# Performance work log

Hardware: AMD Instinct MI355X
Metric: run time of the kernel (lower is better)

## Reference

```python
import jax, jax.numpy as jnp
import numpy as np

N = 50000      # nodes
E = 800000     # edges (avg degree 16)
DIN = 256      # input_dim
DH = 128       # hidden_dim
ALPHA_LOGIT = 0.6190392084062235  # logit(0.65)


def setup_inputs() -> dict:
    key = jax.random.key(0)
    ks = jax.random.split(key, 12)
    f = lambda k, s: jax.random.normal(k, s, dtype=jnp.float32)
    return {
        "x": f(ks[0], (N, DIN)),
        "edge_index": jax.random.randint(ks[1], (2, E), 0, N, dtype=jnp.int32),
        "reranker_scores": f(ks[2], (N,)),
        # input_proj
        "Wp": f(ks[3], (DIN, DH)) * 0.02, "bp": jnp.zeros((DH,), jnp.float32),
        # SAGEConv 0: lin_l (aggregated neighbors, with bias), lin_r (root, no bias)
        "Wl0": f(ks[4], (DIN, DH)) * 0.02, "bl0": jnp.zeros((DH,), jnp.float32),
        "Wr0": f(ks[5], (DIN, DH)) * 0.02,
        # SAGEConv 1
        "Wl1": f(ks[6], (DH, DH)) * 0.02, "bl1": jnp.zeros((DH,), jnp.float32),
        "Wr1": f(ks[7], (DH, DH)) * 0.02,
        # score head MLP
        "W1": f(ks[8], (DH, DH // 2)) * 0.02, "b1": jnp.zeros((DH // 2,), jnp.float32),
        "W2": f(ks[9], (DH // 2, 1)) * 0.02, "b2": jnp.zeros((1,), jnp.float32),
        "alpha_logit": jnp.float32(ALPHA_LOGIT),
    }


def _sage_conv(h, src, dst, Wl, bl, Wr):
    # PyG SAGEConv (aggr='mean', root_weight=True):
    # out = lin_l(mean_{j in N(i)} h_j) + lin_r(h_i)
    msg = h[src]                                             # [E, d] gather
    agg = jax.ops.segment_sum(msg, dst, num_segments=N)      # [N, d]
    cnt = jax.ops.segment_sum(jnp.ones((src.shape[0],), h.dtype), dst, num_segments=N)
    agg = agg / jnp.maximum(cnt, 1.0)[:, None]               # mean; isolated nodes -> 0
    return agg @ Wl + bl + h @ Wr


def reference(x, edge_index, reranker_scores, Wp, bp, Wl0, bl0, Wr0,
              Wl1, bl1, Wr1, W1, b1, W2, b2, alpha_logit):
    src, dst = edge_index[0], edge_index[1]
    # norm_type='none' -> no input normalization; eval mode -> dropout is identity
    residual = x @ Wp + bp                                   # [N, DH]
    h = jax.nn.relu(_sage_conv(x, src, dst, Wl0, bl0, Wr0)) + residual
    h = jax.nn.relu(_sage_conv(h, src, dst, Wl1, bl1, Wr1)) + h
    gnn_scores = (jax.nn.relu(h @ W1 + b1) @ W2 + b2)[:, 0]  # [N]
    alpha = jax.nn.sigmoid(alpha_logit)
    return alpha * reranker_scores + (1.0 - alpha) * gnn_scores
```

## Files before the change

### kernel.cpp

```cpp
#include <hip/hip_runtime.h>
#include <hip/hip_bf16.h>


#define DIN 256
#define DH 128
#define NPB 512
#define NBMAX 128
#define EPB 2048
#define JL (EPB/256)
#define CAP 12288
#define SLOTS 16384

typedef __attribute__((ext_vector_type(8))) short short8;
typedef __attribute__((ext_vector_type(4))) float float4v;
typedef __attribute__((ext_vector_type(2))) float float2v;

__device__ inline ushort f2b(float f){
  unsigned u = __float_as_uint(f);
  u = (u + 0x7fffu + ((u >> 16) & 1u)) >> 16;
  return (ushort)u;
}
__device__ inline float blo(unsigned v){ return __uint_as_float(v << 16); }
__device__ inline float bhi(unsigned v){ return __uint_as_float(v & 0xffff0000u); }
__device__ inline short8 pack8(float4 f0, float4 f1){
  short8 v;
  v[0]=(short)f2b(f0.x); v[1]=(short)f2b(f0.y); v[2]=(short)f2b(f0.z); v[3]=(short)f2b(f0.w);
  v[4]=(short)f2b(f1.x); v[5]=(short)f2b(f1.y); v[6]=(short)f2b(f1.z); v[7]=(short)f2b(f1.w);
  return v;
}
__device__ inline void glds16(const ushort* g, ushort* l){
  __builtin_amdgcn_global_load_lds((const __attribute__((address_space(1))) void*)g,
                                   (__attribute__((address_space(3))) void*)l, 16, 0, 0);
}
__device__ inline unsigned char enc8(float v){
  return (unsigned char)(__builtin_amdgcn_cvt_pk_fp8_f32(v, v, 0, false) & 0xFF);
}
__device__ inline float2v dec8(unsigned u){
  return __builtin_amdgcn_cvt_pk_f32_fp8((int)u, false);
}

__device__ inline void gather16x2(const ushort* __restrict__ a8,
    const int* __restrict__ adj, int pA, int eA, int pB, int eB, int lane,
    float& a0A, float& a1A, float& a0B, float& a1B)
{
  while (pA < eA || pB < eB){
    ushort uA[16], uB[16];
    bool dA = pA < eA, dB = pB < eB;
    if (dA){
      #pragma unroll
      for (int j=0;j<16;j++) uA[j] = a8[(size_t)adj[pA+j]*64 + lane];
    }
    if (dB){
      #pragma unroll
      for (int j=0;j<16;j++) uB[j] = a8[(size_t)adj[pB+j]*64 + lane];
    }
    if (dA){
      #pragma unroll
      for (int j=0;j<16;j++){ float2v f = dec8(uA[j]); a0A += f[0]; a1A += f[1]; }
      pA += 16;
    }
    if (dB){
      #pragma unroll
      for (int j=0;j<16;j++){ float2v f = dec8(uB[j]); a0B += f[0]; a1B += f[1]; }
      pB += 16;
    }
  }
}

__global__ __launch_bounds__(256) void fused_front(
    const float* __restrict__ x, int N, ushort* __restrict__ xb, int nstripe,
    const float* __restrict__ Wp, const float* __restrict__ Wl0, const float* __restrict__ Wr0,
    const float* __restrict__ Wl1, const float* __restrict__ Wr1, const float* __restrict__ W1,
    ushort* __restrict__ Wpf, ushort* __restrict__ Wl0f, ushort* __restrict__ Wr0f,
    ushort* __restrict__ Wl1f, ushort* __restrict__ Wr1f, ushort* __restrict__ W1f,
    const int* __restrict__ src, const int* __restrict__ dst, int E, int NB,
    int* __restrict__ bucketCnt, int* __restrict__ pairS, int* __restrict__ pairD,
    int nPart, int nConv)
{
  __shared__ int hist[NBMAX], lbase[NBMAX], gbase[NBMAX], lcur[NBMAX], sc[NBMAX];
  __shared__ int ls[EPB], ld[EPB];
  int bid = blockIdx.x;
  int t = threadIdx.x;

  if (bid < nPart){
    int base = bid * EPB;
    int cntE = E - base; if (cntE > EPB) cntE = EPB;
    for (int i=t;i<NB;i+=256) hist[i]=0;
    __syncthreads();
    int myS[JL], myD[JL];
    #pragma unroll
    for (int j=0;j<JL;j++){
      int e = base + j*256 + t;
      if (e < E){ myS[j]=src[e]; myD[j]=dst[e]; atomicAdd(&hist[myD[j]>>9],1); }
      else myD[j] = -1;
    }
    __syncthreads();
    if (t < NBMAX) sc[t] = (t < NB)? hist[t] : 0;
    __syncthreads();
    for (int st=1; st<NBMAX; st<<=1){
      int v = 0;
      if (t < NBMAX && t >= st) v = sc[t-st];
      __syncthreads();
      if (t < NBMAX) sc[t] += v;
      __syncthreads();
    }
    if (t < NB){
      int excl = (t>0)? sc[t-1] : 0;
      lbase[t] = excl; lcur[t] = excl;
      gbase[t] = atomicAdd(&bucketCnt[t], hist[t]);
    }
    __syncthreads();
    #pragma unroll
    for (int j=0;j<JL;j++){
      if (myD[j] >= 0){
        int b = myD[j] >> 9;
        int p = atomicAdd(&lcur[b], 1);
        ls[p] = myS[j]; ld[p] = myD[j];
      }
    }
    __syncthreads();
    for (int i=t;i<cntE;i+=256){
      int d = ld[i];
      int b = d >> 9;
      int p = gbase[b] + (i - lbase[b]);
      if (p < SLOTS){
        pairS[(size_t)b*SLOTS + p] = ls[i];
        pairD[(size_t)b*SLOTS + p] = d;
      }
    }
  } else if (bid < nPart + nConv){
    int gi = (bid - nPart)*256 + t;
    if (gi < nstripe*512){
      int L = gi & 63, ks = (gi>>6)&7, s = gi>>9;
      int row = s*16 + (L&15);
      int k = ks*32 + (L>>4)*8;
      short8 v;
      if (row < N){
        const float* p = x + (size_t)row*DIN + k;
        v = pack8(*(const float4*)p, *(const float4*)(p+4));
      } else {
        #pragma unroll
        for (int j=0;j<8;j++) v[j]=0;
      }
      *(short8*)(xb + (size_t)gi*8) = v;
    }
  } else {
    int gi = (bid - nPart - nConv)*256 + t;
    if (gi < 17408){
      const float* sw; ushort* dw; int cols, b0;
      if      (gi <  4096){ sw=Wp;  dw=Wpf;  cols=128; b0=0; }
      else if (gi <  8192){ sw=Wl0; dw=Wl0f; cols=128; b0=4096; }
      else if (gi < 12288){ sw=Wr0; dw=Wr0f; cols=128; b0=8192; }
      else if (gi < 14336){ sw=Wl1; dw=Wl1f; cols=128; b0=12288; }
      else if (gi < 16384){ sw=Wr1; dw=Wr1f; cols=128; b0=14336; }
      else                { sw=W1;  dw=W1f;  cols=64;  b0=16384; }
      int i = gi - b0;
      int ln = i & 63, g = i >> 6;
      int ntq = cols >> 4;
      int nt = g % ntq, ks = g / ntq;
      int col = nt*16 + (ln & 15);
      int k0 = ks*32 + (ln >> 4)*8;
      short8 v;
      #pragma unroll
      for (int j=0;j<8;j++) v[j] = (short)f2b(sw[(size_t)(k0+j)*cols + col]);
      *(short8*)(dw + (size_t)i*8) = v;
    }
  }
}

__global__ __launch_bounds__(256) void gemm0_csr(
    const ushort* __restrict__ xb, int N, int nstripe, int ngemm,
    const ushort* __restrict__ Wpf, const ushort* __restrict__ Wl0f, const ushort* __restrict__ Wr0f,
    const float* __restrict__ bp,
    ushort* __restrict__ xp, unsigned char* __restrict__ q8, ushort* __restrict__ xr0,
    const int* __restrict__ bucketCnt, const int* __restrict__ pairS, const int* __restrict__ pairD,
    int* __restrict__ off, int* __restrict__ deg, int* __restrict__ adj)
{
  __shared__ __align__(16) ushort smem[32768];
  int bid = blockIdx.x, t = threadIdx.x;

  if (bid < ngemm){
    int mat = bid % 3, b = bid / 3;
    int nblk = ngemm / 3;
    const ushort* Wf = (mat==0)? Wpf : (mat==1)? Wl0f : Wr0f;
    int w = t>>6, lane = t&63, lq = lane&15, quad = lane>>4;
    #pragma unroll
    for (int j=0;j<16;j++){
      int g = w + j*4;
      glds16(Wf + (size_t)g*512 + lane*8, smem + g*512);
    }
    __syncthreads();
    float bias[8];
    #pragma unroll
    for (int nt=0;nt<8;nt++) bias[nt] = (mat==0)? bp[nt*16 + lq] : 0.f;
    int nchunk = (nstripe + 3) >> 2;
    for (int c = b; c < nchunk; c += nblk){
      int stripe = c*4 + w;
      int row0 = stripe*16;
      if (row0 >= N) continue;
      short8 av[8];
      #pragma unroll
      for (int ks=0;ks<8;ks++)
        av[ks] = *(const short8*)(xb + ((size_t)stripe*8 + ks)*512 + lane*8);
      float4v acc[8];
      #pragma unroll
      for (int nt=0;nt<8;nt++)
        #pragma unroll
        for (int r=0;r<4;r++) acc[nt][r] = 0.f;
      #pragma unroll
      for (int ks=0;ks<8;ks++){
        #pragma unroll
        for (int nt=0;nt<8;nt++){
          short8 bf = *(const short8*)(smem + (size_t)((ks*8 + nt)*64 + lane)*8);
          acc[nt] = __builtin_amdgcn_mfma_f32_16x16x32_bf16(av[ks], bf, acc[nt], 0,0,0);
        }
      }
      if (mat == 1){
        #pragma unroll
        for (int nt=0;nt<8;nt++)
          #pragma unroll
          for (int r=0;r<4;r++){
            int row = row0 + quad*4 + r;
            if (row < N) q8[(size_t)row*128 + nt*16 + lq] = enc8(acc[nt][r]);
          }
      } else {
        ushort* Y = (mat==0)? xp : xr0;
        #pragma unroll
        for (int nt=0;nt<8;nt++)
          #pragma unroll
          for (int r=0;r<4;r++){
            int row = row0 + quad*4 + r;
            if (row < N) Y[(size_t)row*128 + nt*16 + lq] = f2b(acc[nt][r] + bias[nt]);
          }
      }
    }
  } else {
    int b = bid - ngemm;
    int* cnt  = (int*)smem;
    int* offl = cnt + NPB;
    int* s1   = offl + NPB + 1;
    int* win  = s1 + 256;
    int node0 = b * NPB;
    int base  = b * SLOTS;
    int ce = bucketCnt[b]; if (ce > SLOTS) ce = SLOTS;
    for (int i=t;i<NPB;i+=256) cnt[i]=0;
    __syncthreads();
    for (int i=t;i<ce;i+=256) atomicAdd(&cnt[pairD[(size_t)base+i]-node0], 1);
    __syncthreads();
    int a0 = cnt[2*t], a1 = cnt[2*t+1];
    int p0 = (a0 + 15) & ~15;
    int p1 = (a1 + 15) & ~15;
    s1[t] = p0 + p1;
    __syncthreads();
    for (int st=1; st<256; st<<=1){
      int v = (t>=st)? s1[t-st] : 0;
      __syncthreads();
      s1[t] += v;
      __syncthreads();
    }
    int excl = (t>0)? s1[t-1] : 0;
    offl[2*t] = excl; offl[2*t+1] = excl + p0;
    int ptotal = s1[255]; if (ptotal > SLOTS) ptotal = SLOTS;
    __syncthreads();
    for (int i=t;i<NPB;i+=256){
      int node = node0 + i;
      if (node < N){ off[node] = base + offl[i]; deg[node] = cnt[i]; }
    }
    __syncthreads();
    if (ptotal <= CAP){
      for (int i=t;i<ptotal;i+=256) win[i] = N;
      __syncthreads();
      for (int i=t;i<ce;i+=256){
        int dd = pairD[(size_t)base+i];
        int p = atomicAdd(&offl[dd-node0], 1);
        win[p] = pairS[(size_t)base+i];
      }
      __syncthreads();
      for (int i=t;i<ptotal;i+=256) adj[(size_t)base+i] = win[i];
    } else {
      for (int i=t;i<ptotal;i+=256) adj[(size_t)base+i] = N;
      __syncthreads();
      for (int i=t;i<ce;i+=256){
        int dd = pairD[(size_t)base+i];
        int p = atomicAdd(&offl[dd-node0], 1);
        if (p < SLOTS) adj[(size_t)base+p] = pairS[(size_t)base+i];
      }
    }
  }
}

__global__ __launch_bounds__(256) void combine0_f8(
    const unsigned char* __restrict__ agg8, const ushort* __restrict__ rootsrc,
    const ushort* __restrict__ ressrc, const float* __restrict__ bias,
    const int* __restrict__ off, const int* __restrict__ deg,
    const int* __restrict__ adj, ushort* __restrict__ out, int n)
{
  int t = threadIdx.x;
  int d = t & 63, w = t >> 6;
  int nA = blockIdx.x*8 + w*2, nB = nA + 1;
  if (nA >= n) return;
  const ushort* a8 = (const ushort*)agg8;
  bool vB = nB < n;
  unsigned rtA = ((const unsigned*)rootsrc)[(size_t)nA*64 + d];
  unsigned rsA = ((const unsigned*)ressrc)[(size_t)nA*64 + d];
  unsigned rtB = 0, rsB = 0;
  int pA = off[nA], cA = deg[nA], eA = pA + ((cA + 15) & ~15);
  int pB = 0, cB = 0, eB = 0;
  if (vB){
    rtB = ((const unsigned*)rootsrc)[(size_t)nB*64 + d];
    rsB = ((const unsigned*)ressrc)[(size_t)nB*64 + d];
    pB = off[nB]; cB = deg[nB]; eB = pB + ((cB + 15) & ~15);
  }
  float a0A=0.f, a1A=0.f, a0B=0.f, a1B=0.f;
  gather16x2(a8, adj, pA, eA, pB, eB, d, a0A, a1A, a0B, a1B);
  float b0 = bias[2*d], b1v = bias[2*d+1];
  float invA = 1.f / (float)((cA > 1)? cA : 1);
  float o0 = fmaxf(a0A*invA + b0  + blo(rtA), 0.f) + blo(rsA);
  float o1 = fmaxf(a1A*invA + b1v + bhi(rtA), 0.f) + bhi(rsA);
  ((unsigned*)out)[(size_t)nA*64 + d] = (unsigned)f2b(o0) | ((unsigned)f2b(o1) << 16);
  if (vB){
    float invB = 1.f / (float)((cB > 1)? cB : 1);
    float q0 = fmaxf(a0B*invB + b0  + blo(rtB), 0.f) + blo(rsB);
    float q1 = fmaxf(a1B*invB + b1v + bhi(rtB), 0.f) + bhi(rsB);
    ((unsigned*)out)[(size_t)nB*64 + d] = (unsigned)f2b(q0) | ((unsigned)f2b(q1) << 16);
  }
}

__global__ __launch_bounds__(256) void gemm1_wres(
    const ushort* __restrict__ h, int N,
    const ushort* __restrict__ Wl1f, const ushort* __restrict__ Wr1f,
    unsigned char* __restrict__ q8, ushort* __restrict__ hr1)
{
  __shared__ __align__(16) ushort Bs[32768];
  int t = threadIdx.x, w = t>>6, lane = t&63, lq = lane&15, quad = lane>>4;
  int tile = blockIdx.x;
  #pragma unroll
  for (int j=0;j<16;j++){
    int r = w + j*4;
    int m = r>>5, g = r&31;
    const ushort* Wm = m ? Wr1f : Wl1f;
    glds16(Wm + (size_t)g*512 + lane*8, Bs + r*512);
  }
  short8 av[2][4];
  int row0 = tile*128 + w*32;
  #pragma unroll
  for (int mt=0;mt<2;mt++){
    int row = row0 + mt*16 + lq; if (row >= N) row = N-1;
    #pragma unroll
    for (int ks=0;ks<4;ks++)
      av[mt][ks] = *(const short8*)(h + (size_t)row*128 + ks*32 + quad*8);
  }
  __syncthreads();
  #pragma unroll
  for (int m=0;m<2;m++){
    float4v acc[2][8];
    #pragma unroll
    for (int i=0;i<2;i++)
      #pragma unroll
      for (int j=0;j<8;j++)
        #pragma unroll
        for (int r=0;r<4;r++) acc[i][j][r] = 0.f;
    #pragma unroll
    for (int ks=0;ks<4;ks++){
      #pragma unroll
      for (int nt=0;nt<8;nt++){
        short8 bf = *(const short8*)(Bs + ((m*32 + ks*8 + nt)*64 + lane)*8);
        acc[0][nt] = __builtin_amdgcn_mfma_f32_16x16x32_bf16(av[0][ks], bf, acc[0][nt], 0,0,0);
        acc[1][nt] = __builtin_amdgcn_mfma_f32_16x16x32_bf16(av[1][ks], bf, acc[1][nt], 0,0,0);
      }
    }
    #pragma unroll
    for (int mt=0;mt<2;mt++){
      #pragma unroll
      for (int r=0;r<4;r++){
        int row = row0 + mt*16 + quad*4 + r;
        if (row < N){
          if (m == 0){
            #pragma unroll
            for (int nt=0;nt<8;nt++)
              q8[(size_t)row*128 + nt*16 + lq] = enc8(acc[mt][nt][r]);
          } else {
            #pragma unroll
            for (int nt=0;nt<8;nt++)
              hr1[(size_t)row*128 + nt*16 + lq] = f2b(acc[mt][nt][r]);
          }
        }
      }
    }
  }
}

__global__ __launch_bounds__(256) void combine1_head(
    const unsigned char* __restrict__ agg8, const ushort* __restrict__ hr1,
    const ushort* __restrict__ h, const float* __restrict__ bl1,
    const int* __restrict__ off, const int* __restrict__ deg, const int* __restrict__ adj,
    const ushort* __restrict__ W1f, const float* __restrict__ b1,
    const float* __restrict__ W2, const float* __restrict__ b2,
    const float* __restrict__ alogit, const float* __restrict__ rer,
    float* __restrict__ out, int n)
{
  __shared__ __align__(16) ushort W1s[8192];
  __shared__ __align__(16) ushort h2s[16*136];
  int t = threadIdx.x, w = t>>6, lane = t&63, lq = lane&15, quad = lane>>4;
  #pragma unroll
  for (int j=0;j<4;j++){
    int g = w + j*4;
    glds16(W1f + (size_t)g*512 + lane*8, W1s + g*512);
  }
  int node0 = blockIdx.x*16;
  unsigned* h2u = (unsigned*)h2s;
  const ushort* a8 = (const ushort*)agg8;
  float bb0 = bl1[2*lane], bb1 = bl1[2*lane+1];
  #pragma unroll
  for (int jp=0;jp<2;jp++){
    int nA = node0 + w*4 + jp*2, nB = nA + 1;
    bool vA = nA < n, vB = nB < n;
    unsigned rtA=0, rsA=0, rtB=0, rsB=0;
    int pA=0, eA=0, cA=0, pB=0, eB=0, cB=0;
    if (vA){
      rtA = ((const unsigned*)hr1)[(size_t)nA*64 + lane];
      rsA = ((const unsigned*)h  )[(size_t)nA*64 + lane];
      pA = off[nA]; cA = deg[nA]; eA = pA + ((cA + 15) & ~15);
    }
    if (vB){
      rtB = ((const unsigned*)hr1)[(size_t)nB*64 + lane];
      rsB = ((const unsigned*)h  )[(size_t)nB*64 + lane];
      pB = off[nB]; cB = deg[nB]; eB = pB + ((cB + 15) & ~15);
    }
    float a0A=0.f, a1A=0.f, a0B=0.f, a1B=0.f;
    gather16x2(a8, adj, pA, eA, pB, eB, lane, a0A, a1A, a0B, a1B);
    float o0A=0.f, o1A=0.f, o0B=0.f, o1B=0.f;
    if (vA){
      float inv = 1.f / (float)((cA > 1)? cA : 1);
      o0A = fmaxf(a0A*inv + bb0 + blo(rtA), 0.f) + blo(rsA);
      o1A = fmaxf(a1A*inv + bb1 + bhi(rtA), 0.f) + bhi(rsA);
    }
    if (vB){
      float inv = 1.f / (float)((cB > 1)? cB : 1);
      o0B = fmaxf(a0B*inv + bb0 + blo(rtB), 0.f) + blo(rsB);
      o1B = fmaxf(a1B*inv + bb1 + bhi(rtB), 0.f) + bhi(rsB);
    }
    h2u[(w*4 + jp*2    )*68 + lane] = (unsigned)f2b(o0A) | ((unsigned)f2b(o1A) << 16);
    h2u[(w*4 + jp*2 + 1)*68 + lane] = (unsigned)f2b(o0B) | ((unsigned)f2b(o1B) << 16);
  }
  __syncthreads();

  short8 av[4];
  #pragma unroll
  for (int ks=0;ks<4;ks++)
    av[ks] = *(const short8*)(h2s + lq*136 + ks*32 + quad*8);
  float4v acc[4];
  #pragma unroll
  for (int nt=0;nt<4;nt++)
    #pragma unroll
    for (int r=0;r<4;r++) acc[nt][r] = 0.f;
  #pragma unroll
  for (int ks=0;ks<4;ks++){
    #pragma unroll
    for (int nt=0;nt<4;nt++){
      short8 bf = *(const short8*)(W1s + ((ks*4 + nt)*64 + lane)*8);
      acc[nt] = __builtin_amdgcn_mfma_f32_16x16x32_bf16(av[ks], bf, acc[nt], 0,0,0);
    }
  }
  float al = alogit[0];
  float a  = 1.f / (1.f + __expf(-al));
  float pw[4] = {0.f,0.f,0.f,0.f};
  #pragma unroll
  for (int nt=0; nt<4; nt++){
    int c = nt*16 + lq;
    float w2 = W2[c];
    float bb = b1[c];
    #pragma unroll
    for (int r=0; r<4; r++)
      pw[r] += fmaxf(acc[nt][r] + bb, 0.f) * w2;
  }
  #pragma unroll
  for (int mask=1; mask<16; mask<<=1){
    #pragma unroll
    for (int r=0; r<4; r++)
      pw[r] += __shfl_xor(pw[r], mask);
  }
  if (lq == 0){
    #pragma unroll
    for (int r=0; r<4; r++){
      int rl = quad*4 + r;
      if ((rl >> 2) == w){
        int node = node0 + rl;
        if (node < n)
          out[node] = a * rer[node] + (1.f - a) * (pw[r] + b2[0]);
      }
    }
  }
}

extern "C" void kernel_launch(void* const* d_in, const int* in_sizes, int n_in,
                              void* d_out, int out_size, void* d_ws, size_t ws_size,
                              hipStream_t stream)
{
  (void)n_in; (void)out_size; (void)ws_size;
  const float* x    = (const float*)d_in[0];
  const int*   ei   = (const int*)d_in[1];
  const float* rer  = (const float*)d_in[2];
  const float* Wp   = (const float*)d_in[3];
  const float* bp   = (const float*)d_in[4];
  const float* Wl0  = (const float*)d_in[5];
  const float* bl0  = (const float*)d_in[6];
  const float* Wr0  = (const float*)d_in[7];
  const float* Wl1  = (const float*)d_in[8];
  const float* bl1  = (const float*)d_in[9];
  const float* Wr1  = (const float*)d_in[10];
  const float* W1   = (const float*)d_in[11];
  const float* b1   = (const float*)d_in[12];
  const float* W2   = (const float*)d_in[13];
  const float* b2   = (const float*)d_in[14];
  const float* alogit = (const float*)d_in[15];

  const int N = in_sizes[2];
  const int E = in_sizes[1] / 2;
  const int* src = ei;
  const int* dst = ei + E;
  const int NB = (N + NPB - 1) / NPB;
  const int nstripe = (N + 15) / 16;
  const int ntile = (N + 127) / 128;
  const int nPart = (E + EPB - 1) / EPB;
  const int nConv = (nstripe*512 + 255)/256;

  ushort* U = (ushort*)d_ws;
  ushort* xb  = U;
  ushort* xp  = xb + (size_t)nstripe*512*8;
  ushort* xr0 = xp  + (size_t)N*DH;
  ushort* h   = xr0 + (size_t)N*DH;
  unsigned char* q8 = (unsigned char*)(h + (size_t)N*DH);
  ushort* Wpf  = (ushort*)(q8 + (size_t)(N+1)*DH);
  ushort* Wl0f = Wpf  + (size_t)4096*8;
  ushort* Wr0f = Wl0f + (size_t)4096*8;
  ushort* Wl1f = Wr0f + (size_t)4096*8;
  ushort* Wr1f = Wl1f + (size_t)2048*8;
  ushort* W1f  = Wr1f + (size_t)2048*8;
  int* I = (int*)(W1f + (size_t)1024*8);
  int* bucketCnt = I;
  int* off   = bucketCnt + NBMAX;
  int* deg   = off + N;
  int* pairS = deg + N;
  int* pairD = pairS + (size_t)NB*SLOTS;
  int* adj   = pairD + (size_t)NB*SLOTS;

  hipMemsetAsync(bucketCnt, 0, NBMAX*sizeof(int), stream);
  hipMemsetAsync(q8 + (size_t)N*DH, 0, DH, stream);

  fused_front<<<nPart + nConv + 68, 256, 0, stream>>>(
      x, N, xb, nstripe, Wp, Wl0, Wr0, Wl1, Wr1, W1,
      Wpf, Wl0f, Wr0f, Wl1f, Wr1f, W1f,
      src, dst, E, NB, bucketCnt, pairS, pairD, nPart, nConv);

  gemm0_csr<<<768 + NB, 256, 0, stream>>>(
      xb, N, nstripe, 768, Wpf, Wl0f, Wr0f, bp, xp, q8, xr0,
      bucketCnt, pairS, pairD, off, deg, adj);

  combine0_f8<<<(N+7)/8, 256, 0, stream>>>(q8, xr0, xp, bl0, off, deg, adj, h, N);

  gemm1_wres<<<ntile, 256, 0, stream>>>(h, N, Wl1f, Wr1f, q8, xr0);

  combine1_head<<<(N+15)/16, 256, 0, stream>>>(
      q8, xr0, h, bl1, off, deg, adj, W1f, b1, W2, b2, alogit, rer, (float*)d_out, N);
}
```

Baseline: 250.2 us.

## Halve CSR bucket size, put bucket blocks first, double-buffer gemm0 A loads

Buckets now hold 256 nodes and 8192 slots instead of 512 and 16384, so each CSR-build block has less work and there are twice as many of them. The CSR blocks are moved to the start of the grid so they get scheduled first, and the GEMM blocks are remapped to spread across XCDs. The GEMM loop now prefetches the next stripe's A fragments into a second register buffer while computing the current one, and CSR counting and scatter read pairD and pairS as int4. The added register buffer raises register pressure, and a bucket holding more than 8192 edges would silently drop edges.

```diff
diff --git a/kernel.cpp b/kernel.cpp
--- a/kernel.cpp
+++ b/kernel.cpp
@@ -4,12 +4,12 @@
 
 #define DIN 256
 #define DH 128
-#define NPB 512
-#define NBMAX 128
+#define NPB 256
+#define LOG_NPB 8
+#define NBMAX 256
 #define EPB 2048
 #define JL (EPB/256)
-#define CAP 12288
-#define SLOTS 16384
+#define SLOTS 8192
 
 typedef __attribute__((ext_vector_type(8))) short short8;
 typedef __attribute__((ext_vector_type(4))) float float4v;
@@ -91,7 +91,7 @@
     #pragma unroll
     for (int j=0;j<JL;j++){
       int e = base + j*256 + t;
-      if (e < E){ myS[j]=src[e]; myD[j]=dst[e]; atomicAdd(&hist[myD[j]>>9],1); }
+      if (e < E){ myS[j]=src[e]; myD[j]=dst[e]; atomicAdd(&hist[myD[j]>>LOG_NPB],1); }
       else myD[j] = -1;
     }
     __syncthreads();
@@ -113,7 +113,7 @@
     #pragma unroll
     for (int j=0;j<JL;j++){
       if (myD[j] >= 0){
-        int b = myD[j] >> 9;
+        int b = myD[j] >> LOG_NPB;
         int p = atomicAdd(&lcur[b], 1);
         ls[p] = myS[j]; ld[p] = myD[j];
       }
@@ -121,7 +121,7 @@
     __syncthreads();
     for (int i=t;i<cntE;i+=256){
       int d = ld[i];
-      int b = d >> 9;
+      int b = d >> LOG_NPB;
       int p = gbase[b] + (i - lbase[b]);
       if (p < SLOTS){
         pairS[(size_t)b*SLOTS + p] = ls[i];
@@ -169,7 +169,7 @@
 }
 
 __global__ __launch_bounds__(256) void gemm0_csr(
-    const ushort* __restrict__ xb, int N, int nstripe, int ngemm,
+    const ushort* __restrict__ xb, int N, int nstripe, int ngemm, int nbuck,
     const ushort* __restrict__ Wpf, const ushort* __restrict__ Wl0f, const ushort* __restrict__ Wr0f,
     const float* __restrict__ bp,
     ushort* __restrict__ xp, unsigned char* __restrict__ q8, ushort* __restrict__ xr0,
@@ -179,78 +179,108 @@
   __shared__ __align__(16) ushort smem[32768];
   int bid = blockIdx.x, t = threadIdx.x;
 
-  if (bid < ngemm){
-    int mat = bid % 3, b = bid / 3;
+  if (bid >= nbuck){
+    int g = bid - nbuck;
+    int xcd = g & 7, jj = g >> 3;
+    int mat = jj % 3;
+    int b = xcd + 8*(jj/3);
     int nblk = ngemm / 3;
     const ushort* Wf = (mat==0)? Wpf : (mat==1)? Wl0f : Wr0f;
     int w = t>>6, lane = t&63, lq = lane&15, quad = lane>>4;
     #pragma unroll
     for (int j=0;j<16;j++){
-      int g = w + j*4;
-      glds16(Wf + (size_t)g*512 + lane*8, smem + g*512);
+      int gg = w + j*4;
+      glds16(Wf + (size_t)gg*512 + lane*8, smem + gg*512);
     }
     __syncthreads();
     float bias[8];
     #pragma unroll
     for (int nt=0;nt<8;nt++) bias[nt] = (mat==0)? bp[nt*16 + lq] : 0.f;
     int nchunk = (nstripe + 3) >> 2;
-    for (int c = b; c < nchunk; c += nblk){
-      int stripe = c*4 + w;
-      int row0 = stripe*16;
-      if (row0 >= N) continue;
-      short8 av[8];
-      #pragma unroll
-      for (int ks=0;ks<8;ks++)
-        av[ks] = *(const short8*)(xb + ((size_t)stripe*8 + ks)*512 + lane*8);
-      float4v acc[8];
-      #pragma unroll
-      for (int nt=0;nt<8;nt++)
-        #pragma unroll
-        for (int r=0;r<4;r++) acc[nt][r] = 0.f;
-      #pragma unroll
-      for (int ks=0;ks<8;ks++){
-        #pragma unroll
-        for (int nt=0;nt<8;nt++){
-          short8 bf = *(const short8*)(smem + (size_t)((ks*8 + nt)*64 + lane)*8);
-          acc[nt] = __builtin_amdgcn_mfma_f32_16x16x32_bf16(av[ks], bf, acc[nt], 0,0,0);
-        }
-      }
-      if (mat == 1){
-        #pragma unroll
-        for (int nt=0;nt<8;nt++)
-          #pragma unroll
-          for (int r=0;r<4;r++){
-            int row = row0 + quad*4 + r;
-            if (row < N) q8[(size_t)row*128 + nt*16 + lq] = enc8(acc[nt][r]);
-          }
-      } else {
-        ushort* Y = (mat==0)? xp : xr0;
-        #pragma unroll
-        for (int nt=0;nt<8;nt++)
-          #pragma unroll
-          for (int r=0;r<4;r++){
-            int row = row0 + quad*4 + r;
-            if (row < N) Y[(size_t)row*128 + nt*16 + lq] = f2b(acc[nt][r] + bias[nt]);
-          }
-      }
-    }
+
+#define LOADAV(AV, cc) do { \
+    int stripe_ = (cc)*4 + w; \
+    if (stripe_ < nstripe){ \
+      _Pragma("unroll") \
+      for (int ks=0;ks<8;ks++) \
+        AV[ks] = *(const short8*)(xb + ((size_t)stripe_*8 + ks)*512 + lane*8); \
+    } \
+  } while(0)
+
+#define COMPSTORE(AV, cc) do { \
+    int stripe_ = (cc)*4 + w; \
+    if (stripe_ < nstripe){ \
+      int row0_ = stripe_*16; \
+      float4v acc_[8]; \
+      _Pragma("unroll") for (int nt=0;nt<8;nt++){ \
+        _Pragma("unroll") for (int r=0;r<4;r++) acc_[nt][r]=0.f; } \
+      _Pragma("unroll") for (int ks=0;ks<8;ks++){ \
+        _Pragma("unroll") for (int nt=0;nt<8;nt++){ \
+          short8 bf_ = *(const short8*)(smem + (size_t)((ks*8+nt)*64 + lane)*8); \
+          acc_[nt] = __builtin_amdgcn_mfma_f32_16x16x32_bf16(AV[ks], bf_, acc_[nt], 0,0,0); \
+        } \
+      } \
+      if (mat == 1){ \
+        _Pragma("unroll") for (int nt=0;nt<8;nt++) \
+        _Pragma("unroll") for (int r=0;r<4;r++){ \
+          int row_ = row0_ + quad*4 + r; \
+          if (row_ < N) q8[(size_t)row_*128 + nt*16 + lq] = enc8(acc_[nt][r]); \
+        } \
+      } else { \
+        ushort* Y_ = (mat==0)? xp : xr0; \
+        _Pragma("unroll") for (int nt=0;nt<8;nt++) \
+        _Pragma("unroll") for (int r=0;r<4;r++){ \
+          int row_ = row0_ + quad*4 + r; \
+          if (row_ < N) Y_[(size_t)row_*128 + nt*16 + lq] = f2b(acc_[nt][r] + bias[nt]); \
+        } \
+      } \
+    } \
+  } while(0)
+
+    short8 avA[8], avB[8];
+    int c = b;
+    if (c < nchunk){
+      LOADAV(avA, c);
+      while (true){
+        int cn = c + nblk;
+        if (cn < nchunk) LOADAV(avB, cn);
+        COMPSTORE(avA, c);
+        c = cn;
+        if (c >= nchunk) break;
+        cn = c + nblk;
+        if (cn < nchunk) LOADAV(avA, cn);
+        COMPSTORE(avB, c);
+        c = cn;
+        if (c >= nchunk) break;
+      }
+    }
+#undef LOADAV
+#undef COMPSTORE
   } else {
-    int b = bid - ngemm;
+    int b = bid;
     int* cnt  = (int*)smem;
-    int* offl = cnt + NPB;
-    int* s1   = offl + NPB + 1;
+    int* offl = cnt + 256;
+    int* s1   = offl + 257;
     int* win  = s1 + 256;
     int node0 = b * NPB;
     int base  = b * SLOTS;
     int ce = bucketCnt[b]; if (ce > SLOTS) ce = SLOTS;
-    for (int i=t;i<NPB;i+=256) cnt[i]=0;
-    __syncthreads();
-    for (int i=t;i<ce;i+=256) atomicAdd(&cnt[pairD[(size_t)base+i]-node0], 1);
-    __syncthreads();
-    int a0 = cnt[2*t], a1 = cnt[2*t+1];
-    int p0 = (a0 + 15) & ~15;
-    int p1 = (a1 + 15) & ~15;
-    s1[t] = p0 + p1;
+    int ce4 = ce & ~3;
+    cnt[t] = 0;
+    __syncthreads();
+    for (int i = t*4; i < ce4; i += 1024){
+      int4 dd = *(const int4*)(pairD + base + i);
+      atomicAdd(&cnt[dd.x - node0], 1);
+      atomicAdd(&cnt[dd.y - node0], 1);
+      atomicAdd(&cnt[dd.z - node0], 1);
+      atomicAdd(&cnt[dd.w - node0], 1);
+    }
+    for (int i = ce4 + t; i < ce; i += 256)
+      atomicAdd(&cnt[pairD[(size_t)base+i] - node0], 1);
+    __syncthreads();
+    int a = cnt[t];
+    int pa = (a + 15) & ~15;
+    s1[t] = pa;
     __syncthreads();
     for (int st=1; st<256; st<<=1){
       int v = (t>=st)? s1[t-st] : 0;
@@ -259,33 +289,28 @@
       __syncthreads();
     }
     int excl = (t>0)? s1[t-1] : 0;
-    offl[2*t] = excl; offl[2*t+1] = excl + p0;
+    offl[t] = excl;
     int ptotal = s1[255]; if (ptotal > SLOTS) ptotal = SLOTS;
-    __syncthreads();
-    for (int i=t;i<NPB;i+=256){
-      int node = node0 + i;
-      if (node < N){ off[node] = base + offl[i]; deg[node] = cnt[i]; }
-    }
-    __syncthreads();
-    if (ptotal <= CAP){
-      for (int i=t;i<ptotal;i+=256) win[i] = N;
-      __syncthreads();
-      for (int i=t;i<ce;i+=256){
-        int dd = pairD[(size_t)base+i];
-        int p = atomicAdd(&offl[dd-node0], 1);
-        win[p] = pairS[(size_t)base+i];
-      }
-      __syncthreads();
-      for (int i=t;i<ptotal;i+=256) adj[(size_t)base+i] = win[i];
-    } else {
-      for (int i=t;i<ptotal;i+=256) adj[(size_t)base+i] = N;
-      __syncthreads();
-      for (int i=t;i<ce;i+=256){
-        int dd = pairD[(size_t)base+i];
-        int p = atomicAdd(&offl[dd-node0], 1);
-        if (p < SLOTS) adj[(size_t)base+p] = pairS[(size_t)base+i];
-      }
-    }
+    int node = node0 + t;
+    if (node < N){ off[node] = base + excl; deg[node] = a; }
+    __syncthreads();
+    for (int i=t;i<ptotal;i+=256) win[i] = N;
+    __syncthreads();
+    for (int i = t*4; i < ce4; i += 1024){
+      int4 dd = *(const int4*)(pairD + base + i);
+      int4 ss = *(const int4*)(pairS + base + i);
+      int p0 = atomicAdd(&offl[dd.x - node0], 1); if (p0 < SLOTS) win[p0] = ss.x;
+      int p1 = atomicAdd(&offl[dd.y - node0], 1); if (p1 < SLOTS) win[p1] = ss.y;
+      int p2 = atomicAdd(&offl[dd.z - node0], 1); if (p2 < SLOTS) win[p2] = ss.z;
+      int p3 = atomicAdd(&offl[dd.w - node0], 1); if (p3 < SLOTS) win[p3] = ss.w;
+    }
+    for (int i = ce4 + t; i < ce; i += 256){
+      int dd = pairD[(size_t)base+i];
+      int p = atomicAdd(&offl[dd - node0], 1);
+      if (p < SLOTS) win[p] = pairS[(size_t)base+i];
+    }
+    __syncthreads();
+    for (int i=t;i<ptotal;i+=256) adj[(size_t)base+i] = win[i];
   }
 }
 
@@ -553,8 +578,8 @@
       Wpf, Wl0f, Wr0f, Wl1f, Wr1f, W1f,
       src, dst, E, NB, bucketCnt, pairS, pairD, nPart, nConv);
 
-  gemm0_csr<<<768 + NB, 256, 0, stream>>>(
-      xb, N, nstripe, 768, Wpf, Wl0f, Wr0f, bp, xp, q8, xr0,
+  gemm0_csr<<<NB + 768, 256, 0, stream>>>(
+      xb, N, nstripe, 768, NB, Wpf, Wl0f, Wr0f, bp, xp, q8, xr0,
       bucketCnt, pairS, pairD, off, deg, adj);
 
   combine0_f8<<<(N+7)/8, 256, 0, stream>>>(q8, xr0, xp, bl0, off, deg, adj, h, N);
```

New measurement: 228.0 us. -8.9%, faster.
